# Kernel optimization log

Hardware: AMD Instinct MI355X
Metric: run time of the kernel (lower is better)

## Reference

```python
import jax, jax.numpy as jnp
import numpy as np

NFIELD = 40

def setup_inputs() -> dict:
    key = jax.random.key(0)
    ks = jax.random.split(key, 7)
    B, F, E, A = 1024, NFIELD, 128, 128
    s = 1.0 / np.sqrt(E)
    return {
        "x": jax.random.normal(ks[0], (B, F, E), dtype=jnp.float32),
        "attn_w_w": jax.random.normal(ks[1], (A, E), dtype=jnp.float32) * s,
        "attn_w_b": jax.random.normal(ks[2], (A,), dtype=jnp.float32) * s,
        "attn_h_w": jax.random.normal(ks[3], (1, A), dtype=jnp.float32) * s,
        "attn_h_b": jax.random.normal(ks[4], (1,), dtype=jnp.float32) * s,
        "attn_p_w": jax.random.normal(ks[5], (1, E), dtype=jnp.float32) * s,
        "attn_p_b": jax.random.normal(ks[6], (1,), dtype=jnp.float32) * s,
    }

def reference(x, attn_w_w, attn_w_b, attn_h_w, attn_h_b, attn_p_w, attn_p_b):
    # x: [B, F, E]; pairwise field interactions over upper-triangular (i<j) pairs
    nfield = x.shape[1]
    vi, vj = np.triu_indices(nfield, k=1)  # static index arrays, P = F*(F-1)/2
    hp = x[:, vi, :] * x[:, vj, :]                                   # [B, P, E]
    aw = jax.nn.relu(jnp.einsum('bpe,ae->bpa', hp, attn_w_w) + attn_w_b)  # [B, P, A]
    scores = jnp.einsum('bpa,oa->bpo', aw, attn_h_w) + attn_h_b          # [B, P, 1]
    attn = jax.nn.softmax(scores, axis=1)                                # softmax over pairs
    afm = jnp.sum(attn * hp, axis=1)                                     # [B, E]
    out = jnp.einsum('be,oe->bo', afm, attn_p_w) + attn_p_b              # [B, 1]
    return out.squeeze(1)                                                # [B]
```

## Files before the change

kernel.cpp:

```cpp
#include <hip/hip_runtime.h>
#include <hip/hip_fp16.h>

#define NF 40
#define NE 128
#define NA 128
#define NW 144
#define NP 780
#define NPT 784
#define NMT 49
#define XS16_LD 136

typedef _Float16 half8 __attribute__((ext_vector_type(8)));
typedef float floatx4 __attribute__((ext_vector_type(4)));

__device__ __forceinline__ float rowsum16(float x) {
    x += __int_as_float(__builtin_amdgcn_update_dpp(0, __float_as_int(x), 0x121, 0xf, 0xf, true));
    x += __int_as_float(__builtin_amdgcn_update_dpp(0, __float_as_int(x), 0x122, 0xf, 0xf, true));
    x += __int_as_float(__builtin_amdgcn_update_dpp(0, __float_as_int(x), 0x124, 0xf, 0xf, true));
    x += __int_as_float(__builtin_amdgcn_update_dpp(0, __float_as_int(x), 0x128, 0xf, 0xf, true));
    return x;
}

__global__ __launch_bounds__(256)
void afm_prep_kernel(const float* __restrict__ wg,
                     const float* __restrict__ pwg,
                     unsigned short* __restrict__ wbf,
                     int* __restrict__ ijg)
{
    const int t = blockIdx.x * 256 + threadIdx.x;
    if (t < NW * NE / 4) {
        const int row = t >> 5;
        const int c   = (t & 31) * 4;
        float4 v = make_float4(0.f, 0.f, 0.f, 0.f);
        if (row < NA)       v = *(const float4*)(wg + row * NE + c);
        else if (row == NA) v = *(const float4*)(pwg + c);
        union { _Float16 h[4]; ushort4 u; } cv;
        cv.h[0] = (_Float16)v.x;
        cv.h[1] = (_Float16)v.y;
        cv.h[2] = (_Float16)v.z;
        cv.h[3] = (_Float16)v.w;
        *(ushort4*)(wbf + t * 4) = cv.u;
    }
    if (t < NPT) {
        int v = 0;
        if (t < NP) {
            int i = 0, rem = t;
            while (rem >= (NF - 1 - i)) { rem -= (NF - 1 - i); ++i; }
            v = (i << 8) | (i + 1 + rem);
        }
        ijg[t] = v;
    }
}

__global__ __launch_bounds__(256, 2)
void afm_fused_kernel(const float* __restrict__ xg,
                      const unsigned short* __restrict__ wbf,
                      const int* __restrict__ ijg,
                      const float* __restrict__ wbg,
                      const float* __restrict__ hg,
                      const float* __restrict__ pbg,
                      float* __restrict__ out)
{
    __shared__ unsigned short xs16[NF][XS16_LD];
    __shared__ int   ij[NPT];
    __shared__ float red_n[4], red_d[4];

    const int tid  = threadIdx.x;
    const int b    = blockIdx.x;
    const int lane = tid & 63;
    const int wid  = tid >> 6;
    const int col  = lane & 15;
    const int quad = (lane >> 4) & 3;

    const float* xb = xg + (size_t)b * (NF * NE);
    for (int t = tid; t < NF * (NE / 4); t += 256) {
        int row = t >> 5, c = (t & 31) * 4;
        float4 v = *(const float4*)(xb + row * NE + c);
        union { _Float16 h[4]; unsigned long long ull; } cv;
        cv.h[0] = (_Float16)v.x;
        cv.h[1] = (_Float16)v.y;
        cv.h[2] = (_Float16)v.z;
        cv.h[3] = (_Float16)v.w;
        *(unsigned long long*)&xs16[row][c] = cv.ull;
    }
    if (tid < NPT / 4) {
        *(int4*)&ij[tid * 4] = ((const int4*)ijg)[tid];
    }
    float wbr[8], hr[8];
#pragma unroll
    for (int n = 0; n < 8; ++n) {
        wbr[n] = wbg[n * 16 + col];
        hr[n]  = hg[n * 16 + col];
    }
    half8 bfrag[9][4];
#pragma unroll
    for (int n = 0; n < 9; ++n)
#pragma unroll
        for (int k = 0; k < 4; ++k)
            bfrag[n][k] = *(const half8*)(const void*)(wbf + (n * 16 + col) * NE + k * 32 + quad * 8);
    __syncthreads();

    float nloc = 0.f, dloc = 0.f;
    for (int mt = wid; mt < NMT; mt += 4) {
        const int p0 = mt * 16;
        const int v  = ij[p0 + col];
        const unsigned short* xi16 = &xs16[(v >> 8) & 255][0];
        const unsigned short* xj16 = &xs16[v & 255][0];

        floatx4 acc[9];
#pragma unroll
        for (int n = 0; n < 8; ++n)
            acc[n] = (floatx4){wbr[n], wbr[n], wbr[n], wbr[n]};
        acc[8] = (floatx4){0.f, 0.f, 0.f, 0.f};

#pragma unroll
        for (int k = 0; k < 4; ++k) {
            const int koff = k * 32 + quad * 8;
            half8 ih = *(const half8*)(const void*)(xi16 + koff);
            half8 jh = *(const half8*)(const void*)(xj16 + koff);
            half8 af = ih * jh;
#pragma unroll
            for (int n = 0; n < 9; ++n)
                acc[n] = __builtin_amdgcn_mfma_f32_16x16x32_f16(af, bfrag[n][k], acc[n], 0, 0, 0);
        }

        float ps[4] = {0.f, 0.f, 0.f, 0.f};
#pragma unroll
        for (int n = 0; n < 8; ++n) {
#pragma unroll
            for (int r = 0; r < 4; ++r)
                ps[r] += fmaxf(acc[n][r], 0.f) * hr[n];
        }
#pragma unroll
        for (int r = 0; r < 4; ++r) ps[r] = rowsum16(ps[r]);

#pragma unroll
        for (int r = 0; r < 4; ++r) {
            const int p = p0 + quad * 4 + r;
            const float e = __expf(ps[r]);
            const bool valid = (col == 0) & (p < NP);
            if (valid) {
                nloc += e * acc[8][r];
                dloc += e;
            }
        }
    }
#pragma unroll
    for (int off = 1; off < 64; off <<= 1) {
        nloc += __shfl_xor(nloc, off);
        dloc += __shfl_xor(dloc, off);
    }
    if (lane == 0) { red_n[wid] = nloc; red_d[wid] = dloc; }
    __syncthreads();
    if (tid == 0) {
        float N = red_n[0] + red_n[1] + red_n[2] + red_n[3];
        float D = red_d[0] + red_d[1] + red_d[2] + red_d[3];
        out[b] = N / D + pbg[0];
    }
}

extern "C" void kernel_launch(void* const* d_in, const int* in_sizes, int n_in,
                              void* d_out, int out_size, void* d_ws, size_t ws_size,
                              hipStream_t stream) {
    const float* xg  = (const float*)d_in[0];
    const float* wg  = (const float*)d_in[1];
    const float* wbg = (const float*)d_in[2];
    const float* hg  = (const float*)d_in[3];
    const float* pwg = (const float*)d_in[5];
    const float* pbg = (const float*)d_in[6];
    const int B = in_sizes[0] / (NF * NE);

    unsigned short* wbf = (unsigned short*)d_ws;
    int* ijg = (int*)((char*)d_ws + NW * NE * sizeof(unsigned short));

    afm_prep_kernel<<<20, 256, 0, stream>>>(wg, pwg, wbf, ijg);
    afm_fused_kernel<<<B, 256, 0, stream>>>(xg, wbf, ijg, wbg, hg, pbg, (float*)d_out);
}
```

Measured before the change: 112.3 us.

## Compute pair indices analytically and defer softmax exp to a block-wide pass

Drops the precomputed pair-index table in global memory and its LDS copy. Each lane now recovers (i,j) from the pair id with a sqrt-based closed form plus correction steps. Per-tile scores and pooled values are written to a shared float2 buffer, and after a barrier all threads compute exp and accumulate numerator and denominator in parallel, replacing the single-column-lane exp path. The MFMA loop is also wrapped in s_setprio to raise wave priority. In exchange it adds extra ALU work for the index math, an extra barrier, and more LDS.

```diff
diff --git a/kernel.cpp b/kernel.cpp
--- a/kernel.cpp
+++ b/kernel.cpp
@@ -24,8 +24,7 @@
 __global__ __launch_bounds__(256)
 void afm_prep_kernel(const float* __restrict__ wg,
                      const float* __restrict__ pwg,
-                     unsigned short* __restrict__ wbf,
-                     int* __restrict__ ijg)
+                     unsigned short* __restrict__ wbf)
 {
     const int t = blockIdx.x * 256 + threadIdx.x;
     if (t < NW * NE / 4) {
@@ -41,28 +40,18 @@
         cv.h[3] = (_Float16)v.w;
         *(ushort4*)(wbf + t * 4) = cv.u;
     }
-    if (t < NPT) {
-        int v = 0;
-        if (t < NP) {
-            int i = 0, rem = t;
-            while (rem >= (NF - 1 - i)) { rem -= (NF - 1 - i); ++i; }
-            v = (i << 8) | (i + 1 + rem);
-        }
-        ijg[t] = v;
-    }
 }
 
 __global__ __launch_bounds__(256, 2)
 void afm_fused_kernel(const float* __restrict__ xg,
                       const unsigned short* __restrict__ wbf,
-                      const int* __restrict__ ijg,
                       const float* __restrict__ wbg,
                       const float* __restrict__ hg,
                       const float* __restrict__ pbg,
                       float* __restrict__ out)
 {
     __shared__ unsigned short xs16[NF][XS16_LD];
-    __shared__ int   ij[NPT];
+    __shared__ float2 scq[NPT];
     __shared__ float red_n[4], red_d[4];
 
     const int tid  = threadIdx.x;
@@ -83,9 +72,6 @@
         cv.h[3] = (_Float16)v.w;
         *(unsigned long long*)&xs16[row][c] = cv.ull;
     }
-    if (tid < NPT / 4) {
-        *(int4*)&ij[tid * 4] = ((const int4*)ijg)[tid];
-    }
     float wbr[8], hr[8];
 #pragma unroll
     for (int n = 0; n < 8; ++n) {
@@ -100,12 +86,19 @@
             bfrag[n][k] = *(const half8*)(const void*)(wbf + (n * 16 + col) * NE + k * 32 + quad * 8);
     __syncthreads();
 
-    float nloc = 0.f, dloc = 0.f;
     for (int mt = wid; mt < NMT; mt += 4) {
         const int p0 = mt * 16;
-        const int v  = ij[p0 + col];
-        const unsigned short* xi16 = &xs16[(v >> 8) & 255][0];
-        const unsigned short* xj16 = &xs16[v & 255][0];
+        int p = p0 + col;
+        if (p > NP - 1) p = NP - 1;
+        float sq = sqrtf((float)(6241 - 8 * p));
+        int i  = (int)((79.0f - sq) * 0.5f);
+        int rsb = (i * (79 - i)) >> 1;
+        int rsn = ((i + 1) * (78 - i)) >> 1;
+        if (rsn <= p) { i += 1; rsb = rsn; }
+        if (rsb > p)  { i -= 1; rsb = (i * (79 - i)) >> 1; }
+        const int j = i + 1 + (p - rsb);
+        const unsigned short* xi16 = &xs16[i][0];
+        const unsigned short* xj16 = &xs16[j][0];
 
         floatx4 acc[9];
 #pragma unroll
@@ -113,6 +106,7 @@
             acc[n] = (floatx4){wbr[n], wbr[n], wbr[n], wbr[n]};
         acc[8] = (floatx4){0.f, 0.f, 0.f, 0.f};
 
+        __builtin_amdgcn_s_setprio(1);
 #pragma unroll
         for (int k = 0; k < 4; ++k) {
             const int koff = k * 32 + quad * 8;
@@ -123,6 +117,7 @@
             for (int n = 0; n < 9; ++n)
                 acc[n] = __builtin_amdgcn_mfma_f32_16x16x32_f16(af, bfrag[n][k], acc[n], 0, 0, 0);
         }
+        __builtin_amdgcn_s_setprio(0);
 
         float ps[4] = {0.f, 0.f, 0.f, 0.f};
 #pragma unroll
@@ -134,16 +129,22 @@
 #pragma unroll
         for (int r = 0; r < 4; ++r) ps[r] = rowsum16(ps[r]);
 
+        if (col == 0) {
 #pragma unroll
-        for (int r = 0; r < 4; ++r) {
-            const int p = p0 + quad * 4 + r;
-            const float e = __expf(ps[r]);
-            const bool valid = (col == 0) & (p < NP);
-            if (valid) {
-                nloc += e * acc[8][r];
-                dloc += e;
+            for (int r = 0; r < 4; ++r) {
+                const int pp = p0 + quad * 4 + r;
+                scq[pp] = make_float2(ps[r], acc[8][r]);
             }
         }
+    }
+    __syncthreads();
+
+    float nloc = 0.f, dloc = 0.f;
+    for (int p = tid; p < NP; p += 256) {
+        float2 v = scq[p];
+        float e = __expf(v.x);
+        nloc += e * v.y;
+        dloc += e;
     }
 #pragma unroll
     for (int off = 1; off < 64; off <<= 1) {
@@ -171,8 +172,7 @@
     const int B = in_sizes[0] / (NF * NE);
 
     unsigned short* wbf = (unsigned short*)d_ws;
-    int* ijg = (int*)((char*)d_ws + NW * NE * sizeof(unsigned short));
 
-    afm_prep_kernel<<<20, 256, 0, stream>>>(wg, pwg, wbf, ijg);
-    afm_fused_kernel<<<B, 256, 0, stream>>>(xg, wbf, ijg, wbg, hg, pbg, (float*)d_out);
+    afm_prep_kernel<<<18, 256, 0, stream>>>(wg, pwg, wbf);
+    afm_fused_kernel<<<B, 256, 0, stream>>>(xg, wbf, wbg, hg, pbg, (float*)d_out);
 }
```

After: 114.3 us. No clear change (+1.8%).
